# Kernel optimization log

Hardware: AMD Instinct MI355X
Metric: run time of the kernel (lower is better)

## Reference

```python
import jax, jax.numpy as jnp
import numpy as np
import math

FEATURE_DIMS = [32, 64, 96, 128, 192, 256, 384, 512]
HIDDEN = 128
BATCH = 32768


def setup_inputs() -> dict:
    key = jax.random.key(0)
    keys = jax.random.split(key, 2 * len(FEATURE_DIMS) + len(FEATURE_DIMS) + 1)
    inp = {}
    # feature tensors (batch, dim_i)
    for i, d in enumerate(FEATURE_DIMS):
        inp[f"feat{i}"] = jax.random.normal(keys[i], (BATCH, d), dtype=jnp.float32)
    # per-feature key/value projection weights, torch nn.Linear layout (hidden, dim)
    n = len(FEATURE_DIMS)
    for i, d in enumerate(FEATURE_DIMS):
        bound = 1.0 / math.sqrt(d)
        inp[f"Wk{i}"] = jax.random.uniform(keys[n + i], (HIDDEN, d), dtype=jnp.float32, minval=-bound, maxval=bound)
        inp[f"Wv{i}"] = jax.random.uniform(keys[2 * n + i], (HIDDEN, d), dtype=jnp.float32, minval=-bound, maxval=bound)
    inp["query"] = jax.random.normal(keys[-1], (HIDDEN,), dtype=jnp.float32)
    return inp


def reference(feat0, feat1, feat2, feat3, feat4, feat5, feat6, feat7,
              Wk0, Wk1, Wk2, Wk3, Wk4, Wk5, Wk6, Wk7,
              Wv0, Wv1, Wv2, Wv3, Wv4, Wv5, Wv6, Wv7,
              query):
    feats = [feat0, feat1, feat2, feat3, feat4, feat5, feat6, feat7]
    Wks = [Wk0, Wk1, Wk2, Wk3, Wk4, Wk5, Wk6, Wk7]
    Wvs = [Wv0, Wv1, Wv2, Wv3, Wv4, Wv5, Wv6, Wv7]
    # per-feature projections: x @ W.T, torch Linear(bias=False) semantics
    K = jnp.stack([jnp.einsum('bd,hd->bh', f, W) for f, W in zip(feats, Wks)], axis=1)  # (B, F, H)
    V = jnp.stack([jnp.einsum('bd,hd->bh', f, W) for f, W in zip(feats, Wvs)], axis=1)  # (B, F, H)
    scores = jnp.einsum('bfh,h->bf', K, query) / math.sqrt(HIDDEN)  # (B, F)
    attn_weights = jax.nn.softmax(scores, axis=-1)
    combined = jnp.einsum('bf,bfh->bh', attn_weights, V)  # (B, H)
    # dropout is identity in eval mode
    return combined, attn_weights
```

## Files before the change

### kernel.cpp

```cpp
#include <hip/hip_runtime.h>
#include <hip/hip_bf16.h>

#define THREADS 256
#define MTILE   32
#define HID     128
#define BATCH   32768
#define NFEAT   8
#define SDMAX   264

typedef __attribute__((ext_vector_type(4))) float f32x4;
typedef __attribute__((ext_vector_type(8))) short s16x8;

struct Ptrs {
    const float* feat[NFEAT];
    const float* wk[NFEAT];
    const float* wv[NFEAT];
    const float* q;
};

__device__ __forceinline__ float bf2f(unsigned short u) {
    union { unsigned int i; float f; } c; c.i = ((unsigned int)u) << 16; return c.f;
}
__device__ __forceinline__ unsigned short f2bf(float f) {
    union { __hip_bfloat16 h; unsigned short u; } c; c.h = __float2bfloat16(f); return c.u;
}

__device__ const int g_fdim[NFEAT] = {32, 64, 96, 128, 192, 256, 384, 512};
__device__ const int g_foff[NFEAT] = {0, 32, 96, 192, 320, 512, 768, 1152};

__global__ void prep_qk(Ptrs p, float* qk) {
    int i = blockIdx.x;
    int d = g_fdim[i];
    const float* Wk = p.wk[i];
    const float* q  = p.q;
    for (int c = threadIdx.x; c < d; c += blockDim.x) {
        float s = 0.f;
        #pragma unroll 8
        for (int h = 0; h < HID; ++h) s = fmaf(q[h], Wk[h * d + c], s);
        qk[g_foff[i] + c] = s * 0.08838834764831845f;
    }
}

__global__ void prep_wv(Ptrs p, unsigned short* WvB) {
    int fi    = blockIdx.x >> 3;
    int slice = blockIdx.x & 7;
    int D  = g_fdim[fi];
    int Dg = D >> 3;
    const float* Wv = p.wv[fi];
    unsigned short* out = WvB + 128 * g_foff[fi];
    int h0  = slice * 16;
    int cnt = 16 * Dg;
    for (int e = threadIdx.x; e < cnt; e += blockDim.x) {
        int h  = h0 + e / Dg;
        int kg = e - (e / Dg) * Dg;
        const float* src = Wv + h * D + kg * 8;
        float4 x = *reinterpret_cast<const float4*>(src);
        float4 y = *reinterpret_cast<const float4*>(src + 4);
        s16x8 b;
        b[0] = (short)f2bf(x.x); b[1] = (short)f2bf(x.y);
        b[2] = (short)f2bf(x.z); b[3] = (short)f2bf(x.w);
        b[4] = (short)f2bf(y.x); b[5] = (short)f2bf(y.y);
        b[6] = (short)f2bf(y.z); b[7] = (short)f2bf(y.w);
        *reinterpret_cast<s16x8*>(out + (kg * 128 + h) * 8) = b;
    }
}

template<int FI, int D, int CK0, int DC>
__device__ __forceinline__ void stage_issue(const Ptrs& p, int row0, int tid, float4* regs) {
    const float* fbase = p.feat[FI] + (size_t)row0 * D + CK0;
    constexpr int NITER = (MTILE * DC / 4) / THREADS;
    #pragma unroll
    for (int jj = 0; jj < NITER; ++jj) {
        int flat = (tid + jj * THREADS) * 4;
        int r = flat / DC;
        int c = flat - r * DC;
        regs[jj] = *reinterpret_cast<const float4*>(fbase + (size_t)r * D + c);
    }
}

template<int DC>
__device__ __forceinline__ void stage_commit(const float4* regs, unsigned short* A, int tid) {
    constexpr int SD = DC + 8;
    constexpr int NITER = (MTILE * DC / 4) / THREADS;
    #pragma unroll
    for (int jj = 0; jj < NITER; ++jj) {
        int flat = (tid + jj * THREADS) * 4;
        int r = flat / DC;
        int c = flat - r * DC;
        float4 v = regs[jj];
        ushort4 u;
        u.x = f2bf(v.x); u.y = f2bf(v.y); u.z = f2bf(v.z); u.w = f2bf(v.w);
        *reinterpret_cast<ushort4*>(&A[r * SD + c]) = u;
    }
}

template<int FI, int FOFF, int CK0, int DC, bool FIRST, bool LAST>
__device__ __forceinline__ void compute_chunk(
    const unsigned short* A, const unsigned short* WvB, const float* qk,
    float* wAll, float* Zrow, float& spart,
    f32x4 (&P)[2][2], f32x4 (&O)[2][2],
    int tid, int wave, int l15, int q4)
{
    constexpr int SD = DC + 8;
    if (FIRST) {
        spart = 0.f;
        #pragma unroll
        for (int mt = 0; mt < 2; ++mt) {
            P[mt][0] = f32x4{0.f, 0.f, 0.f, 0.f};
            P[mt][1] = f32x4{0.f, 0.f, 0.f, 0.f};
        }
    }

    {
        int r = tid >> 3, part = tid & 7;
        constexpr int Q = DC / 8;
        const float* qf = qk + FOFF + CK0 + part * Q;
        const unsigned short* arow = A + r * SD + part * Q;
        float acc = 0.f;
        #pragma unroll
        for (int c = 0; c < Q; c += 4) {
            ushort4 u  = *reinterpret_cast<const ushort4*>(arow + c);
            float4  qv = *reinterpret_cast<const float4*>(qf + c);
            acc += bf2f(u.x) * qv.x + bf2f(u.y) * qv.y +
                   bf2f(u.z) * qv.z + bf2f(u.w) * qv.w;
        }
        spart += acc;
    }

    {
        const unsigned short* Wb = WvB + 128 * FOFF;
        #pragma unroll
        for (int kk = 0; kk < DC / 32; ++kk) {
            int kg = CK0 / 8 + kk * 4 + q4;
            int hb = wave * 32 + l15;
            s16x8 b0 = *reinterpret_cast<const s16x8*>(Wb + (kg * 128 + hb) * 8);
            s16x8 b1 = *reinterpret_cast<const s16x8*>(Wb + (kg * 128 + hb + 16) * 8);
            int k0 = kk * 32 + q4 * 8;
            #pragma unroll
            for (int mt = 0; mt < 2; ++mt) {
                s16x8 a = *reinterpret_cast<const s16x8*>(A + (mt * 16 + l15) * SD + k0);
                P[mt][0] = __builtin_amdgcn_mfma_f32_16x16x32_bf16(a, b0, P[mt][0], 0, 0, 0);
                P[mt][1] = __builtin_amdgcn_mfma_f32_16x16x32_bf16(a, b1, P[mt][1], 0, 0, 0);
            }
        }
    }

    if (LAST) {
        float s = spart;
        s += __shfl_xor(s, 1, 64);
        s += __shfl_xor(s, 2, 64);
        s += __shfl_xor(s, 4, 64);
        int r = tid >> 3;
        if ((tid & 7) == 0) {
            float w = __expf(s);
            wAll[FI * MTILE + r] = w;
            Zrow[r] += w;
        }
        __syncthreads();
        #pragma unroll
        for (int mt = 0; mt < 2; ++mt) {
            #pragma unroll
            for (int rr = 0; rr < 4; ++rr) {
                float w = wAll[FI * MTILE + mt * 16 + q4 * 4 + rr];
                O[mt][0][rr] += w * P[mt][0][rr];
                O[mt][1][rr] += w * P[mt][1][rr];
            }
        }
    }
}

__global__ __launch_bounds__(THREADS, 4)
void attn_main(Ptrs p, const unsigned short* WvB, const float* qk,
               float* outC, float* outA) {
    __shared__ __align__(16) unsigned short Abuf[2 * MTILE * SDMAX];
    __shared__ float wAll[NFEAT * MTILE];
    __shared__ float Zrow[MTILE];
    unsigned short* buf0 = Abuf;
    unsigned short* buf1 = Abuf + MTILE * SDMAX;

    int tid  = threadIdx.x;
    int wave = tid >> 6;
    int lane = tid & 63;
    int l15  = lane & 15, q4 = lane >> 4;
    int row0 = blockIdx.x * MTILE;

    if (tid < MTILE) Zrow[tid] = 0.f;

    f32x4 P[2][2], O[2][2];
    #pragma unroll
    for (int mt = 0; mt < 2; ++mt) {
        O[mt][0] = f32x4{0.f, 0.f, 0.f, 0.f};
        O[mt][1] = f32x4{0.f, 0.f, 0.f, 0.f};
    }
    float spart = 0.f;
    float4 regs[8];

#define ISSUE(FI,D,CK0,DC)                stage_issue<FI,D,CK0,DC>(p, row0, tid, regs)
#define COMMIT(DC,BUF)                    stage_commit<DC>(regs, BUF, tid)
#define COMP(FI,FOFF,CK0,DC,FIRST,LAST,BUF) \
    compute_chunk<FI,FOFF,CK0,DC,FIRST,LAST>(BUF, WvB, qk, wAll, Zrow, spart, P, O, tid, wave, l15, q4)

    ISSUE(0,  32,   0,  32);                                          COMMIT( 32, buf0); __syncthreads();
    ISSUE(1,  64,   0,  64); COMP(0,    0,   0,  32, true,  true,  buf0); COMMIT( 64, buf1); __syncthreads();
    ISSUE(2,  96,   0,  96); COMP(1,   32,   0,  64, true,  true,  buf1); COMMIT( 96, buf0); __syncthreads();
    ISSUE(3, 128,   0, 128); COMP(2,   96,   0,  96, true,  true,  buf0); COMMIT(128, buf1); __syncthreads();
    ISSUE(4, 192,   0, 192); COMP(3,  192,   0, 128, true,  true,  buf1); COMMIT(192, buf0); __syncthreads();
    ISSUE(5, 256,   0, 256); COMP(4,  320,   0, 192, true,  true,  buf0); COMMIT(256, buf1); __syncthreads();
    ISSUE(6, 384,   0, 256); COMP(5,  512,   0, 256, true,  true,  buf1); COMMIT(256, buf0); __syncthreads();
    ISSUE(6, 384, 256, 128); COMP(6,  768,   0, 256, true,  false, buf0); COMMIT(128, buf1); __syncthreads();
    ISSUE(7, 512,   0, 256); COMP(6,  768, 256, 128, false, true,  buf1); COMMIT(256, buf0); __syncthreads();
    ISSUE(7, 512, 256, 256); COMP(7, 1152,   0, 256, true,  false, buf0); COMMIT(256, buf1); __syncthreads();
                             COMP(7, 1152, 256, 256, false, true,  buf1);

    __syncthreads();
    float* Ctmp = reinterpret_cast<float*>(Abuf);
    #pragma unroll
    for (int mt = 0; mt < 2; ++mt) {
        #pragma unroll
        for (int rr = 0; rr < 4; ++rr) {
            int row = mt * 16 + q4 * 4 + rr;
            float zi = 1.0f / Zrow[row];
            Ctmp[row * 136 + wave * 32 + l15]      = O[mt][0][rr] * zi;
            Ctmp[row * 136 + wave * 32 + 16 + l15] = O[mt][1][rr] * zi;
        }
    }
    __syncthreads();
    #pragma unroll
    for (int it = 0; it < 4; ++it) {
        int j = tid + it * THREADS;
        int r = j >> 5, c4 = (j & 31) * 4;
        *reinterpret_cast<float4*>(outC + (size_t)(row0 + r) * HID + c4) =
            *reinterpret_cast<const float4*>(Ctmp + r * 136 + c4);
    }
    if (tid < MTILE) {
        float zi = 1.0f / Zrow[tid];
        float4 a0, a1;
        a0.x = wAll[0 * MTILE + tid] * zi; a0.y = wAll[1 * MTILE + tid] * zi;
        a0.z = wAll[2 * MTILE + tid] * zi; a0.w = wAll[3 * MTILE + tid] * zi;
        a1.x = wAll[4 * MTILE + tid] * zi; a1.y = wAll[5 * MTILE + tid] * zi;
        a1.z = wAll[6 * MTILE + tid] * zi; a1.w = wAll[7 * MTILE + tid] * zi;
        float* dst = outA + (size_t)(row0 + tid) * NFEAT;
        *reinterpret_cast<float4*>(dst)     = a0;
        *reinterpret_cast<float4*>(dst + 4) = a1;
    }
#undef ISSUE
#undef COMMIT
#undef COMP
}

extern "C" void kernel_launch(void* const* d_in, const int* in_sizes, int n_in,
                              void* d_out, int out_size, void* d_ws, size_t ws_size,
                              hipStream_t stream) {
    Ptrs p;
    for (int i = 0; i < NFEAT; ++i) {
        p.feat[i] = (const float*)d_in[i];
        p.wk[i]   = (const float*)d_in[NFEAT + 2 * i];
        p.wv[i]   = (const float*)d_in[NFEAT + 2 * i + 1];
    }
    p.q = (const float*)d_in[3 * NFEAT];

    unsigned short* WvB = (unsigned short*)d_ws;
    float* qk = (float*)((char*)d_ws + 128 * 1664 * 2);

    prep_wv<<<NFEAT * 8, 256, 0, stream>>>(p, WvB);
    prep_qk<<<NFEAT, 256, 0, stream>>>(p, qk);

    float* outC = (float*)d_out;
    float* outA = outC + (size_t)BATCH * HID;
    attn_main<<<BATCH / MTILE, THREADS, 0, stream>>>(p, WvB, qk, outC, outA);
}
```

Measured before the change: 349.3 us.

## Stage features into LDS via direct global-to-LDS DMA with XOR swizzle

Replaces the register-staged load, bf16 convert and LDS store of feature tiles with global_load_lds DMA that writes fp32 directly into a swizzled LDS layout, converting to bf16 at fragment-load time. Chunks are cut to at most 128 columns so the double buffer fits the fp32 layout. The per-feature barrier inside the weight fold is removed by deferring the fold to the next stage, and the normaliser is computed once at the end. This trims register pressure and the per-stage store and sync cost, at the price of more stages, doubled LDS traffic for fp32 reads, and conversion work inside the MFMA loop.

Measured after the change: 353.3 us. No clear change (+1.1%).

```diff
diff --git a/kernel.cpp b/kernel.cpp
--- a/kernel.cpp
+++ b/kernel.cpp
@@ -6,10 +6,12 @@
 #define HID     128
 #define BATCH   32768
 #define NFEAT   8
-#define SDMAX   264
 
 typedef __attribute__((ext_vector_type(4))) float f32x4;
 typedef __attribute__((ext_vector_type(8))) short s16x8;
+
+typedef unsigned int __attribute__((address_space(1))) as1_u32;
+typedef unsigned int __attribute__((address_space(3))) as3_u32;
 
 struct Ptrs {
     const float* feat[NFEAT];
@@ -18,11 +20,12 @@
     const float* q;
 };
 
-__device__ __forceinline__ float bf2f(unsigned short u) {
-    union { unsigned int i; float f; } c; c.i = ((unsigned int)u) << 16; return c.f;
-}
 __device__ __forceinline__ unsigned short f2bf(float f) {
     union { __hip_bfloat16 h; unsigned short u; } c; c.h = __float2bfloat16(f); return c.u;
+}
+
+__device__ __forceinline__ void dma16(const float* g, float* l) {
+    __builtin_amdgcn_global_load_lds((const as1_u32*)g, (as3_u32*)l, 16, 0, 0);
 }
 
 __device__ const int g_fdim[NFEAT] = {32, 64, 96, 128, 192, 256, 384, 512};
@@ -65,43 +68,28 @@
     }
 }
 
-template<int FI, int D, int CK0, int DC>
-__device__ __forceinline__ void stage_issue(const Ptrs& p, int row0, int tid, float4* regs) {
-    const float* fbase = p.feat[FI] + (size_t)row0 * D + CK0;
-    constexpr int NITER = (MTILE * DC / 4) / THREADS;
-    #pragma unroll
-    for (int jj = 0; jj < NITER; ++jj) {
-        int flat = (tid + jj * THREADS) * 4;
-        int r = flat / DC;
-        int c = flat - r * DC;
-        regs[jj] = *reinterpret_cast<const float4*>(fbase + (size_t)r * D + c);
-    }
-}
-
-template<int DC>
-__device__ __forceinline__ void stage_commit(const float4* regs, unsigned short* A, int tid) {
-    constexpr int SD = DC + 8;
-    constexpr int NITER = (MTILE * DC / 4) / THREADS;
-    #pragma unroll
-    for (int jj = 0; jj < NITER; ++jj) {
-        int flat = (tid + jj * THREADS) * 4;
-        int r = flat / DC;
-        int c = flat - r * DC;
-        float4 v = regs[jj];
-        ushort4 u;
-        u.x = f2bf(v.x); u.y = f2bf(v.y); u.z = f2bf(v.z); u.w = f2bf(v.w);
-        *reinterpret_cast<ushort4*>(&A[r * SD + c]) = u;
-    }
-}
-
-template<int FI, int FOFF, int CK0, int DC, bool FIRST, bool LAST>
+template<int FI, int D, int CK0, int DC, int MASK>
+__device__ __forceinline__ void stage(const Ptrs& p, int row0, int tid, float* buf) {
+    const float* fp = p.feat[FI];
+    constexpr int NIT = DC / 32;
+    #pragma unroll
+    for (int it = 0; it < NIT; ++it) {
+        int e4 = it * THREADS + tid;
+        int e  = e4 * 4;
+        int r  = e / DC;
+        int cp = e - r * DC;
+        int gl = (cp >> 3) ^ (r & MASK);
+        int col = CK0 + gl * 8 + (cp & 7);
+        dma16(fp + (size_t)(row0 + r) * D + col, buf + e);
+    }
+}
+
+template<int FI, int FOFF, int CK0, int DC, int MASK, bool FIRST, bool LAST>
 __device__ __forceinline__ void compute_chunk(
-    const unsigned short* A, const unsigned short* WvB, const float* qk,
-    float* wAll, float* Zrow, float& spart,
-    f32x4 (&P)[2][2], f32x4 (&O)[2][2],
+    const float* buf, const unsigned short* WvB, const float* qk,
+    float* wAll, float& spart, f32x4 (&P)[2][2],
     int tid, int wave, int l15, int q4)
 {
-    constexpr int SD = DC + 8;
     if (FIRST) {
         spart = 0.f;
         #pragma unroll
@@ -113,34 +101,49 @@
 
     {
         int r = tid >> 3, part = tid & 7;
-        constexpr int Q = DC / 8;
-        const float* qf = qk + FOFF + CK0 + part * Q;
-        const unsigned short* arow = A + r * SD + part * Q;
+        constexpr int G = DC / 8;
         float acc = 0.f;
         #pragma unroll
-        for (int c = 0; c < Q; c += 4) {
-            ushort4 u  = *reinterpret_cast<const ushort4*>(arow + c);
-            float4  qv = *reinterpret_cast<const float4*>(qf + c);
-            acc += bf2f(u.x) * qv.x + bf2f(u.y) * qv.y +
-                   bf2f(u.z) * qv.z + bf2f(u.w) * qv.w;
+        for (int gi = 0; gi < G; gi += 8) {
+            int g = gi + part;
+            if (g < G) {
+                int gp = g ^ (r & MASK);
+                const float* a = buf + r * DC + gp * 8;
+                float4 u0 = *reinterpret_cast<const float4*>(a);
+                float4 u1 = *reinterpret_cast<const float4*>(a + 4);
+                const float* qf = qk + FOFF + CK0 + g * 8;
+                float4 q0 = *reinterpret_cast<const float4*>(qf);
+                float4 q1 = *reinterpret_cast<const float4*>(qf + 4);
+                acc += u0.x*q0.x + u0.y*q0.y + u0.z*q0.z + u0.w*q0.w
+                     + u1.x*q1.x + u1.y*q1.y + u1.z*q1.z + u1.w*q1.w;
+            }
         }
         spart += acc;
     }
 
     {
-        const unsigned short* Wb = WvB + 128 * FOFF;
+        int hb = wave * 32 + l15;
         #pragma unroll
         for (int kk = 0; kk < DC / 32; ++kk) {
-            int kg = CK0 / 8 + kk * 4 + q4;
-            int hb = wave * 32 + l15;
-            s16x8 b0 = *reinterpret_cast<const s16x8*>(Wb + (kg * 128 + hb) * 8);
-            s16x8 b1 = *reinterpret_cast<const s16x8*>(Wb + (kg * 128 + hb + 16) * 8);
-            int k0 = kk * 32 + q4 * 8;
+            int kgG = CK0 / 8 + kk * 4 + q4;
+            const unsigned short* bb = WvB + 128 * FOFF + ((size_t)kgG * 128 + hb) * 8;
+            s16x8 b0 = *reinterpret_cast<const s16x8*>(bb);
+            s16x8 b1 = *reinterpret_cast<const s16x8*>(bb + 128);
+            int glA = kk * 4 + q4;
             #pragma unroll
             for (int mt = 0; mt < 2; ++mt) {
-                s16x8 a = *reinterpret_cast<const s16x8*>(A + (mt * 16 + l15) * SD + k0);
-                P[mt][0] = __builtin_amdgcn_mfma_f32_16x16x32_bf16(a, b0, P[mt][0], 0, 0, 0);
-                P[mt][1] = __builtin_amdgcn_mfma_f32_16x16x32_bf16(a, b1, P[mt][1], 0, 0, 0);
+                int m = mt * 16 + l15;
+                int gp = glA ^ (m & MASK);
+                const float* a = buf + m * DC + gp * 8;
+                float4 x = *reinterpret_cast<const float4*>(a);
+                float4 y = *reinterpret_cast<const float4*>(a + 4);
+                s16x8 af;
+                af[0] = (short)f2bf(x.x); af[1] = (short)f2bf(x.y);
+                af[2] = (short)f2bf(x.z); af[3] = (short)f2bf(x.w);
+                af[4] = (short)f2bf(y.x); af[5] = (short)f2bf(y.y);
+                af[6] = (short)f2bf(y.z); af[7] = (short)f2bf(y.w);
+                P[mt][0] = __builtin_amdgcn_mfma_f32_16x16x32_bf16(af, b0, P[mt][0], 0, 0, 0);
+                P[mt][1] = __builtin_amdgcn_mfma_f32_16x16x32_bf16(af, b1, P[mt][1], 0, 0, 0);
             }
         }
     }
@@ -150,21 +153,20 @@
         s += __shfl_xor(s, 1, 64);
         s += __shfl_xor(s, 2, 64);
         s += __shfl_xor(s, 4, 64);
-        int r = tid >> 3;
-        if ((tid & 7) == 0) {
-            float w = __expf(s);
-            wAll[FI * MTILE + r] = w;
-            Zrow[r] += w;
-        }
-        __syncthreads();
-        #pragma unroll
-        for (int mt = 0; mt < 2; ++mt) {
-            #pragma unroll
-            for (int rr = 0; rr < 4; ++rr) {
-                float w = wAll[FI * MTILE + mt * 16 + q4 * 4 + rr];
-                O[mt][0][rr] += w * P[mt][0][rr];
-                O[mt][1][rr] += w * P[mt][1][rr];
-            }
+        if ((tid & 7) == 0)
+            wAll[FI * MTILE + (tid >> 3)] = __expf(s);
+    }
+}
+
+template<int FI>
+__device__ __forceinline__ void fold(const float* wAll, f32x4 (&P)[2][2], f32x4 (&O)[2][2], int q4) {
+    #pragma unroll
+    for (int mt = 0; mt < 2; ++mt) {
+        #pragma unroll
+        for (int rr = 0; rr < 4; ++rr) {
+            float w = wAll[FI * MTILE + mt * 16 + q4 * 4 + rr];
+            O[mt][0][rr] += w * P[mt][0][rr];
+            O[mt][1][rr] += w * P[mt][1][rr];
         }
     }
 }
@@ -172,11 +174,11 @@
 __global__ __launch_bounds__(THREADS, 4)
 void attn_main(Ptrs p, const unsigned short* WvB, const float* qk,
                float* outC, float* outA) {
-    __shared__ __align__(16) unsigned short Abuf[2 * MTILE * SDMAX];
+    __shared__ __align__(16) float Abuf[2 * MTILE * 128];
     __shared__ float wAll[NFEAT * MTILE];
     __shared__ float Zrow[MTILE];
-    unsigned short* buf0 = Abuf;
-    unsigned short* buf1 = Abuf + MTILE * SDMAX;
+    float* buf0 = Abuf;
+    float* buf1 = Abuf + MTILE * 128;
 
     int tid  = threadIdx.x;
     int wave = tid >> 6;
@@ -184,8 +186,6 @@
     int l15  = lane & 15, q4 = lane >> 4;
     int row0 = blockIdx.x * MTILE;
 
-    if (tid < MTILE) Zrow[tid] = 0.f;
-
     f32x4 P[2][2], O[2][2];
     #pragma unroll
     for (int mt = 0; mt < 2; ++mt) {
@@ -193,47 +193,59 @@
         O[mt][1] = f32x4{0.f, 0.f, 0.f, 0.f};
     }
     float spart = 0.f;
-    float4 regs[8];
-
-#define ISSUE(FI,D,CK0,DC)                stage_issue<FI,D,CK0,DC>(p, row0, tid, regs)
-#define COMMIT(DC,BUF)                    stage_commit<DC>(regs, BUF, tid)
-#define COMP(FI,FOFF,CK0,DC,FIRST,LAST,BUF) \
-    compute_chunk<FI,FOFF,CK0,DC,FIRST,LAST>(BUF, WvB, qk, wAll, Zrow, spart, P, O, tid, wave, l15, q4)
-
-    ISSUE(0,  32,   0,  32);                                          COMMIT( 32, buf0); __syncthreads();
-    ISSUE(1,  64,   0,  64); COMP(0,    0,   0,  32, true,  true,  buf0); COMMIT( 64, buf1); __syncthreads();
-    ISSUE(2,  96,   0,  96); COMP(1,   32,   0,  64, true,  true,  buf1); COMMIT( 96, buf0); __syncthreads();
-    ISSUE(3, 128,   0, 128); COMP(2,   96,   0,  96, true,  true,  buf0); COMMIT(128, buf1); __syncthreads();
-    ISSUE(4, 192,   0, 192); COMP(3,  192,   0, 128, true,  true,  buf1); COMMIT(192, buf0); __syncthreads();
-    ISSUE(5, 256,   0, 256); COMP(4,  320,   0, 192, true,  true,  buf0); COMMIT(256, buf1); __syncthreads();
-    ISSUE(6, 384,   0, 256); COMP(5,  512,   0, 256, true,  true,  buf1); COMMIT(256, buf0); __syncthreads();
-    ISSUE(6, 384, 256, 128); COMP(6,  768,   0, 256, true,  false, buf0); COMMIT(128, buf1); __syncthreads();
-    ISSUE(7, 512,   0, 256); COMP(6,  768, 256, 128, false, true,  buf1); COMMIT(256, buf0); __syncthreads();
-    ISSUE(7, 512, 256, 256); COMP(7, 1152,   0, 256, true,  false, buf0); COMMIT(256, buf1); __syncthreads();
-                             COMP(7, 1152, 256, 256, false, true,  buf1);
-
-    __syncthreads();
-    float* Ctmp = reinterpret_cast<float*>(Abuf);
+
+#define STG(FI,D,CK0,DC,MASK,BUF)  stage<FI,D,CK0,DC,MASK>(p, row0, tid, BUF)
+#define CMP(FI,FOFF,CK0,DC,MASK,FIRST,LAST,BUF) \
+    compute_chunk<FI,FOFF,CK0,DC,MASK,FIRST,LAST>(BUF, WvB, qk, wAll, spart, P, tid, wave, l15, q4)
+#define FOLD(FI) fold<FI>(wAll, P, O, q4)
+#define BAR() __syncthreads()
+
+    STG(0, 32,   0, 32,3, buf0);                        BAR();
+    STG(1, 64,   0, 64,7, buf1);          CMP(0,   0,   0, 32,3,true ,true , buf0); BAR();
+    STG(2, 96,   0, 96,3, buf0); FOLD(0); CMP(1,  32,   0, 64,7,true ,true , buf1); BAR();
+    STG(3,128,   0,128,7, buf1); FOLD(1); CMP(2,  96,   0, 96,3,true ,true , buf0); BAR();
+    STG(4,192,   0,128,7, buf0); FOLD(2); CMP(3, 192,   0,128,7,true ,true , buf1); BAR();
+    STG(4,192, 128, 64,7, buf1); FOLD(3); CMP(4, 320,   0,128,7,true ,false, buf0); BAR();
+    STG(5,256,   0,128,7, buf0);          CMP(4, 320, 128, 64,7,false,true , buf1); BAR();
+    STG(5,256, 128,128,7, buf1); FOLD(4); CMP(5, 512,   0,128,7,true ,false, buf0); BAR();
+    STG(6,384,   0,128,7, buf0);          CMP(5, 512, 128,128,7,false,true , buf1); BAR();
+    STG(6,384, 128,128,7, buf1); FOLD(5); CMP(6, 768,   0,128,7,true ,false, buf0); BAR();
+    STG(6,384, 256,128,7, buf0);          CMP(6, 768, 128,128,7,false,false, buf1); BAR();
+    STG(7,512,   0,128,7, buf1);          CMP(6, 768, 256,128,7,false,true , buf0); BAR();
+    STG(7,512, 128,128,7, buf0); FOLD(6); CMP(7,1152,   0,128,7,true ,false, buf1); BAR();
+    STG(7,512, 256,128,7, buf1);          CMP(7,1152, 128,128,7,false,false, buf0); BAR();
+    STG(7,512, 384,128,7, buf0);          CMP(7,1152, 256,128,7,false,false, buf1); BAR();
+                                          CMP(7,1152, 384,128,7,false,true , buf0); BAR();
+    FOLD(7);
+    if (tid < MTILE) {
+        float z = 0.f;
+        #pragma unroll
+        for (int f = 0; f < NFEAT; ++f) z += wAll[f * MTILE + tid];
+        Zrow[tid] = 1.0f / z;
+    }
+    BAR();
+
+    float* Ctmp = Abuf;
     #pragma unroll
     for (int mt = 0; mt < 2; ++mt) {
         #pragma unroll
         for (int rr = 0; rr < 4; ++rr) {
             int row = mt * 16 + q4 * 4 + rr;
-            float zi = 1.0f / Zrow[row];
-            Ctmp[row * 136 + wave * 32 + l15]      = O[mt][0][rr] * zi;
-            Ctmp[row * 136 + wave * 32 + 16 + l15] = O[mt][1][rr] * zi;
-        }
-    }
-    __syncthreads();
+            float zi = Zrow[row];
+            Ctmp[row * 132 + wave * 32 + l15]      = O[mt][0][rr] * zi;
+            Ctmp[row * 132 + wave * 32 + 16 + l15] = O[mt][1][rr] * zi;
+        }
+    }
+    BAR();
     #pragma unroll
     for (int it = 0; it < 4; ++it) {
         int j = tid + it * THREADS;
         int r = j >> 5, c4 = (j & 31) * 4;
         *reinterpret_cast<float4*>(outC + (size_t)(row0 + r) * HID + c4) =
-            *reinterpret_cast<const float4*>(Ctmp + r * 136 + c4);
+            *reinterpret_cast<const float4*>(Ctmp + r * 132 + c4);
     }
     if (tid < MTILE) {
-        float zi = 1.0f / Zrow[tid];
+        float zi = Zrow[tid];
         float4 a0, a1;
         a0.x = wAll[0 * MTILE + tid] * zi; a0.y = wAll[1 * MTILE + tid] * zi;
         a0.z = wAll[2 * MTILE + tid] * zi; a0.w = wAll[3 * MTILE + tid] * zi;
@@ -243,9 +255,10 @@
         *reinterpret_cast<float4*>(dst)     = a0;
         *reinterpret_cast<float4*>(dst + 4) = a1;
     }
-#undef ISSUE
-#undef COMMIT
-#undef COMP
+#undef STG
+#undef CMP
+#undef FOLD
+#undef BAR
 }
 
 extern "C" void kernel_launch(void* const* d_in, const int* in_sizes, int n_in,
```
